# Optimization experiments

Hardware: AMD Instinct MI355X
Metric: run time of the kernel (lower is better)

## Reference

```python
import jax, jax.numpy as jnp
import numpy as np

N = 40000          # nodes
E = 640000         # edges
D_IN, D_HID, D_EMB, D_OUT = 128, 128, 64, 2


def glorot(key, shape):
    lim = np.sqrt(6.0 / (shape[0] + shape[1]))
    return jax.random.uniform(key, shape, jnp.float32, -lim, lim)


def setup_inputs() -> dict:
    key = jax.random.key(0)
    ks = jax.random.split(key, 8)
    x = jax.random.normal(ks[0], (N, D_IN), jnp.float32)
    edge_index = jax.random.randint(ks[1], (2, E), 0, N, dtype=jnp.int64)
    # GCNConv weights stored as [in, out]; biases zero-init per PyG default
    W1 = glorot(ks[2], (D_IN, D_HID));  b1 = jnp.zeros((D_HID,), jnp.float32)
    W2 = glorot(ks[3], (D_HID, D_HID)); b2 = jnp.zeros((D_HID,), jnp.float32)
    W3 = glorot(ks[4], (D_HID, D_EMB)); b3 = jnp.zeros((D_EMB,), jnp.float32)
    Wout = glorot(ks[5], (D_EMB, D_OUT)); bout = jnp.zeros((D_OUT,), jnp.float32)
    return {"x": x, "edge_index": edge_index,
            "W1": W1, "b1": b1, "W2": W2, "b2": b2,
            "W3": W3, "b3": b3, "Wout": Wout, "bout": bout}


def _gcn_norm(edge_index, n):
    # add self loops, compute symmetric normalization d^-1/2[src] * d^-1/2[dst]
    loop = jnp.arange(n, dtype=edge_index.dtype)
    src = jnp.concatenate([edge_index[0], loop])
    dst = jnp.concatenate([edge_index[1], loop])
    deg = jax.ops.segment_sum(jnp.ones_like(dst, dtype=jnp.float32), dst,
                              num_segments=n)
    dinv = jax.lax.rsqrt(deg)                      # deg >= 1 due to self-loops
    dinv = jnp.where(jnp.isinf(dinv), 0.0, dinv)
    return src, dst, dinv[src] * dinv[dst]


def gcn_conv(x, src, dst, norm, W, b):
    h = x @ W                                      # [N, out]
    msg = h[src] * norm[:, None]                   # gather + scale  [E+N, out]
    return jax.ops.segment_sum(msg, dst, num_segments=x.shape[0]) + b


def reference(x, edge_index, W1, b1, W2, b2, W3, b3, Wout, bout):
    n = x.shape[0]
    src, dst, norm = _gcn_norm(edge_index, n)      # cached=True: computed once
    h = jax.nn.relu(gcn_conv(x, src, dst, norm, W1, b1))   # dropout is identity in eval
    h = jax.nn.relu(gcn_conv(h, src, dst, norm, W2, b2))
    h = gcn_conv(h, src, dst, norm, W3, b3)
    out = h @ Wout + bout
    return (out, h)
```

## Files before the change

kernel.cpp:

```cpp
#include <hip/hip_runtime.h>
#include <hip/hip_bf16.h>

#define NN 40000
#define NE 640000

typedef unsigned int u32;
typedef unsigned short u16;
typedef __attribute__((ext_vector_type(8))) short bf16x8;
typedef __attribute__((ext_vector_type(4))) float f32x4;

__device__ float g_wf[512];
__device__ u16   g_wp[40960];
__device__ int   g_cnt[NN];
__device__ int   g_cur[NN];
__device__ int   g_rowptr[NN + 1];
__device__ float g_dinv[NN];
__device__ int   g_csrc[NE];
__device__ int   g_bsum[64];
__device__ u16   g_ha[(size_t)NN * 128];
__device__ u16   g_hb[(size_t)NN * 128];
__device__ u16   g_hb2[(size_t)NN * 128];

#define OFF_B1 0
#define OFF_B2 128
#define OFF_B3 256
#define OFF_WO 320
#define OFF_BO 448
#define WP_W1 0
#define WP_W2 16384
#define WP_W3 32768

__device__ __forceinline__ float b2f(u16 v){ return __uint_as_float(((u32)v) << 16); }
__device__ __forceinline__ float blo(u32 u){ return __uint_as_float(u << 16); }
__device__ __forceinline__ float bhi(u32 u){ return __uint_as_float(u & 0xffff0000u); }
__device__ __forceinline__ u32 f2bf(float f){
  u32 u = __float_as_uint(f);
  return (u + 0x7fffu + ((u >> 16) & 1u)) >> 16;
}
__device__ __forceinline__ int clampi(int v, int lo, int hi){ return v < lo ? lo : (v > hi ? hi : v); }
__device__ __forceinline__ u16 ldbf(const void* p, int idx, int f32){
  return f32 ? (u16)f2bf(((const float*)p)[idx]) : ((const u16*)p)[idx];
}
__device__ __forceinline__ float ldf(const void* p, int idx, int f32){
  return f32 ? ((const float*)p)[idx] : b2f(((const u16*)p)[idx]);
}

__device__ __forceinline__ int detect_xf32(const u16* __restrict__ xf){
  int i = ((int)threadIdx.x & 63) * 64;
  u16 v = xf[2 * i];
  int e = (v >> 7) & 0xff;
  int pass = (v == 0 || (e >= 100 && e <= 140)) ? 1 : 0;
  return (__popcll(__ballot(pass)) < 32) ? 1 : 0;
}
__device__ __forceinline__ int detect_estride(const int* __restrict__ ei){
  int i = ((int)threadIdx.x & 63) * 64;
  int pass = (ei[2 * i + 1] == 0) ? 1 : 0;
  return (__popcll(__ballot(pass)) >= 32) ? 2 : 1;
}

__global__ __launch_bounds__(256) void k_prep(const void* xin, const int* __restrict__ ei,
                                              const void* w1, const void* b1,
                                              const void* w2, const void* b2, const void* w3,
                                              const void* b3, const void* wo, const void* bo){
  int xf32 = detect_xf32((const u16*)xin);
  int strd = detect_estride(ei);
  int T = (int)blockIdx.x * 256 + (int)threadIdx.x;
  if (T < 640000){
    if (xf32){
      const float4* p = (const float4*)xin + (size_t)T * 2;
      float4 a = p[0], b = p[1];
      uint4 o;
      o.x = f2bf(a.x) | (f2bf(a.y) << 16);
      o.y = f2bf(a.z) | (f2bf(a.w) << 16);
      o.z = f2bf(b.x) | (f2bf(b.y) << 16);
      o.w = f2bf(b.z) | (f2bf(b.w) << 16);
      ((uint4*)g_ha)[T] = o;
    } else {
      ((uint4*)g_ha)[T] = ((const uint4*)xin)[T];
    }
    int d = clampi(ei[(size_t)(NE + T) * strd], 0, NN - 1);
    atomicAdd(&g_cnt[d], 1);
  } else if (T < 680960){
    int local = T - 640000;
    int J, dstbase, l; const void* src;
    if (local < 16384){ J = 128; src = w1; dstbase = WP_W1; l = local; }
    else if (local < 32768){ J = 128; src = w2; dstbase = WP_W2; l = local - 16384; }
    else { J = 64; src = w3; dstbase = WP_W3; l = local - 32768; }
    int chunk = l >> 9, within = l & 511;
    int nbw = J / 16;
    int kb = chunk / nbw, nb = chunk % nbw;
    int lane = within >> 3, j = within & 7;
    int q = lane >> 4, n = lane & 15;
    int k = kb * 32 + q * 8 + j;
    int col = nb * 16 + n;
    g_wp[dstbase + l] = ldbf(src, k * J + col, xf32);
  } else if (T < 681410){
    int l = T - 680960;
    if (l < 128)      g_wf[OFF_B1 + l] = ldf(b1, l, xf32);
    else if (l < 256) g_wf[OFF_B2 + l - 128] = ldf(b2, l - 128, xf32);
    else if (l < 320) g_wf[OFF_B3 + l - 256] = ldf(b3, l - 256, xf32);
    else if (l < 448) g_wf[OFF_WO + l - 320] = ldf(wo, l - 320, xf32);
    else              g_wf[OFF_BO + l - 448] = ldf(bo, l - 448, xf32);
  }
}

__global__ __launch_bounds__(1024) void k_scan1(){
  int t = (int)threadIdx.x;
  int b = (int)blockIdx.x;
  int i = b * 1024 + t;
  int v = (i < NN) ? g_cnt[i] : 0;
  int lane = t & 63, wv = t >> 6;
  int x = v;
#pragma unroll
  for (int ofs = 1; ofs < 64; ofs <<= 1){
    int y = __shfl_up(x, ofs, 64);
    if (lane >= ofs) x += y;
  }
  __shared__ int wsum[16];
  if (lane == 63) wsum[wv] = x;
  __syncthreads();
  if (t < 16){
    int s = wsum[t];
#pragma unroll
    for (int ofs = 1; ofs < 16; ofs <<= 1){
      int y = __shfl_up(s, ofs, 64);
      if (t >= ofs) s += y;
    }
    wsum[t] = s;
  }
  __syncthreads();
  int pre = (wv == 0) ? 0 : wsum[wv - 1];
  int incl = x + pre;
  if (i < NN){
    g_rowptr[i] = incl - v;
    g_dinv[i] = rsqrtf((float)(v + 1));
  }
  if (t == 1023) g_bsum[b] = incl;
}

__global__ __launch_bounds__(1024) void k_scan3(){
  __shared__ int pre;
  int t = (int)threadIdx.x;
  if (t < 64){
    int v = (t < 40) ? g_bsum[t] : 0;
    int s = v;
#pragma unroll
    for (int ofs = 1; ofs < 64; ofs <<= 1){
      int y = __shfl_up(s, ofs, 64);
      if (t >= ofs) s += y;
    }
    if (t == (int)blockIdx.x) pre = s - v;
    if (blockIdx.x == 0 && t == 39) g_rowptr[NN] = s;
  }
  __syncthreads();
  int i = (int)blockIdx.x * 1024 + t;
  if (i < NN) g_rowptr[i] += pre;
}

__global__ __launch_bounds__(256) void k_fillgemm(const int* __restrict__ ei){
  int bid = (int)blockIdx.x;
  if (bid < 2500){
    int strd = detect_estride(ei);
    int e = bid * 256 + (int)threadIdx.x;
    if (e < NE){
      int d = clampi(ei[(size_t)(NE + e) * strd], 0, NN - 1);
      int s = clampi(ei[(size_t)e * strd], 0, NN - 1);
      int pos = clampi(g_rowptr[d] + atomicAdd(&g_cur[d], 1), 0, NE - 1);
      g_csrc[pos] = s;
    }
  } else {
    constexpr int J = 128;
    constexpr int NB = J / 16;
    int tid = (int)threadIdx.x;
    int wave = tid >> 6, lane = tid & 63;
    int q = lane >> 4, n = lane & 15;
    int m0 = (bid - 2500) * 64 + wave * 16;
    f32x4 acc[NB];
#pragma unroll
    for (int nb = 0; nb < NB; ++nb) acc[nb] = (f32x4){0.f, 0.f, 0.f, 0.f};
    const u16* arow = g_ha + (size_t)(m0 + n) * 128 + q * 8;
#pragma unroll
    for (int kb = 0; kb < 4; ++kb){
      bf16x8 a = *(const bf16x8*)(arow + kb * 32);
      const u16* wbase = g_wp + WP_W1 + (kb * NB) * 512 + lane * 8;
#pragma unroll
      for (int nb = 0; nb < NB; ++nb){
        bf16x8 w = *(const bf16x8*)(wbase + nb * 512);
        acc[nb] = __builtin_amdgcn_mfma_f32_16x16x32_bf16(a, w, acc[nb], 0, 0, 0);
      }
    }
    u16* crow = g_hb + (size_t)(m0 + q * 4) * J + n;
#pragma unroll
    for (int r = 0; r < 4; ++r){
      float di = g_dinv[m0 + q * 4 + r];
#pragma unroll
      for (int nb = 0; nb < NB; ++nb)
        crow[(size_t)r * J + nb * 16] = (u16)f2bf(acc[nb][r] * di);
    }
  }
}

#define ACC8(P) do { \
    a0 += blo((P).x); a1 += bhi((P).x); \
    a2 += blo((P).y); a3 += bhi((P).y); \
    a4 += blo((P).z); a5 += bhi((P).z); \
    a6 += blo((P).w); a7 += bhi((P).w); } while (0)

template<int JOUT, bool SWAP, bool ZCLR>
__global__ __launch_bounds__(256, 4) void k_agggemm(int boff, int wpoff){
  constexpr int LSTRIDE = 136;
  __shared__ u16 tile[16 * LSTRIDE];
  const u16* __restrict__ src = SWAP ? g_hb2 : g_hb;
  u16* __restrict__ dst = SWAP ? g_hb : g_hb2;
  int tid = (int)threadIdx.x;
  int gt = (int)blockIdx.x * 256 + tid;
  if (ZCLR){ if (gt < NN){ g_cnt[gt] = 0; g_cur[gt] = 0; } }
  int wid = gt >> 4;
  int rt = tid >> 4;
  int lane = tid & 15;
  int cc = lane * 8;
  float di = g_dinv[wid];
  int beg = g_rowptr[wid], end = g_rowptr[wid + 1];
  uint4 ps = *(const uint4*)(src + (size_t)wid * 128 + cc);
  float a0 = 0.f, a1 = 0.f, a2 = 0.f, a3 = 0.f, a4 = 0.f, a5 = 0.f, a6 = 0.f, a7 = 0.f;
  for (int e = beg; e < end; e += 8){
    int s0, s1, s2, s3, s4, s5, s6, s7;
    {
      int last = end - 1;
#define LDS_IDX(T) clampi(g_csrc[(e + T < last) ? (e + T) : last], 0, NN - 1)
      s0 = LDS_IDX(0); s1 = LDS_IDX(1); s2 = LDS_IDX(2); s3 = LDS_IDX(3);
      s4 = LDS_IDX(4); s5 = LDS_IDX(5); s6 = LDS_IDX(6); s7 = LDS_IDX(7);
#undef LDS_IDX
    }
    uint4 p0 = *(const uint4*)(src + (size_t)s0 * 128 + cc);
    uint4 p1 = *(const uint4*)(src + (size_t)s1 * 128 + cc);
    uint4 p2 = *(const uint4*)(src + (size_t)s2 * 128 + cc);
    uint4 p3 = *(const uint4*)(src + (size_t)s3 * 128 + cc);
    uint4 p4 = *(const uint4*)(src + (size_t)s4 * 128 + cc);
    uint4 p5 = *(const uint4*)(src + (size_t)s5 * 128 + cc);
    uint4 p6 = *(const uint4*)(src + (size_t)s6 * 128 + cc);
    uint4 p7 = *(const uint4*)(src + (size_t)s7 * 128 + cc);
    int nv = end - e;
    ACC8(p0);
    if (nv > 1) ACC8(p1);
    if (nv > 2) ACC8(p2);
    if (nv > 3) ACC8(p3);
    if (nv > 4) ACC8(p4);
    if (nv > 5) ACC8(p5);
    if (nv > 6) ACC8(p6);
    if (nv > 7) ACC8(p7);
  }
  ACC8(ps);
  a0 = a0 * di + g_wf[boff + cc];
  a1 = a1 * di + g_wf[boff + cc + 1];
  a2 = a2 * di + g_wf[boff + cc + 2];
  a3 = a3 * di + g_wf[boff + cc + 3];
  a4 = a4 * di + g_wf[boff + cc + 4];
  a5 = a5 * di + g_wf[boff + cc + 5];
  a6 = a6 * di + g_wf[boff + cc + 6];
  a7 = a7 * di + g_wf[boff + cc + 7];
  a0 = fmaxf(a0, 0.f); a1 = fmaxf(a1, 0.f); a2 = fmaxf(a2, 0.f); a3 = fmaxf(a3, 0.f);
  a4 = fmaxf(a4, 0.f); a5 = fmaxf(a5, 0.f); a6 = fmaxf(a6, 0.f); a7 = fmaxf(a7, 0.f);
  {
    uint4 o;
    o.x = f2bf(a0) | (f2bf(a1) << 16);
    o.y = f2bf(a2) | (f2bf(a3) << 16);
    o.z = f2bf(a4) | (f2bf(a5) << 16);
    o.w = f2bf(a6) | (f2bf(a7) << 16);
    *(uint4*)&tile[rt * LSTRIDE + cc] = o;
  }
  __syncthreads();
  constexpr int NBF = JOUT / 16;
  constexpr int NBW = NBF / 4;
  int wave = tid >> 6, l64 = tid & 63;
  int q = l64 >> 4, n = l64 & 15;
  f32x4 acc[NBW];
#pragma unroll
  for (int j = 0; j < NBW; ++j) acc[j] = (f32x4){0.f, 0.f, 0.f, 0.f};
#pragma unroll
  for (int kb = 0; kb < 4; ++kb){
    bf16x8 a = *(const bf16x8*)&tile[n * LSTRIDE + q * 8 + kb * 32];
#pragma unroll
    for (int j = 0; j < NBW; ++j){
      int nb = wave * NBW + j;
      bf16x8 w = *(const bf16x8*)(g_wp + wpoff + (kb * NBF + nb) * 512 + l64 * 8);
      acc[j] = __builtin_amdgcn_mfma_f32_16x16x32_bf16(a, w, acc[j], 0, 0, 0);
    }
  }
  int m0 = (int)blockIdx.x * 16;
#pragma unroll
  for (int r = 0; r < 4; ++r){
    float dr = g_dinv[m0 + q * 4 + r];
#pragma unroll
    for (int j = 0; j < NBW; ++j){
      int nb = wave * NBW + j;
      dst[(size_t)(m0 + q * 4 + r) * JOUT + nb * 16 + n] = (u16)f2bf(acc[j][r] * dr);
    }
  }
}

template<int J, bool RELU>
__global__ __launch_bounds__(256, 4) void k_agg(int boff, float* __restrict__ h3, float* __restrict__ outp){
  constexpr int LPR = J / 8;
  int gt = (int)blockIdx.x * 256 + (int)threadIdx.x;
  int wid = gt / LPR;
  int lane = (int)threadIdx.x & (LPR - 1);
  if (wid >= NN) return;
  int cc = lane * 8;
  const u16* __restrict__ hb = g_hb;
  float di = g_dinv[wid];
  int beg = g_rowptr[wid], end = g_rowptr[wid + 1];
  uint4 ps = *(const uint4*)(hb + (size_t)wid * J + cc);
  float a0 = 0.f, a1 = 0.f, a2 = 0.f, a3 = 0.f, a4 = 0.f, a5 = 0.f, a6 = 0.f, a7 = 0.f;
  for (int e = beg; e < end; e += 8){
    int s0, s1, s2, s3, s4, s5, s6, s7;
    {
      int last = end - 1;
#define LDS_IDX(T) clampi(g_csrc[(e + T < last) ? (e + T) : last], 0, NN - 1)
      s0 = LDS_IDX(0); s1 = LDS_IDX(1); s2 = LDS_IDX(2); s3 = LDS_IDX(3);
      s4 = LDS_IDX(4); s5 = LDS_IDX(5); s6 = LDS_IDX(6); s7 = LDS_IDX(7);
#undef LDS_IDX
    }
    uint4 p0 = *(const uint4*)(hb + (size_t)s0 * J + cc);
    uint4 p1 = *(const uint4*)(hb + (size_t)s1 * J + cc);
    uint4 p2 = *(const uint4*)(hb + (size_t)s2 * J + cc);
    uint4 p3 = *(const uint4*)(hb + (size_t)s3 * J + cc);
    uint4 p4 = *(const uint4*)(hb + (size_t)s4 * J + cc);
    uint4 p5 = *(const uint4*)(hb + (size_t)s5 * J + cc);
    uint4 p6 = *(const uint4*)(hb + (size_t)s6 * J + cc);
    uint4 p7 = *(const uint4*)(hb + (size_t)s7 * J + cc);
    int nv = end - e;
    ACC8(p0);
    if (nv > 1) ACC8(p1);
    if (nv > 2) ACC8(p2);
    if (nv > 3) ACC8(p3);
    if (nv > 4) ACC8(p4);
    if (nv > 5) ACC8(p5);
    if (nv > 6) ACC8(p6);
    if (nv > 7) ACC8(p7);
  }
  ACC8(ps);
  a0 = a0 * di + g_wf[boff + cc];
  a1 = a1 * di + g_wf[boff + cc + 1];
  a2 = a2 * di + g_wf[boff + cc + 2];
  a3 = a3 * di + g_wf[boff + cc + 3];
  a4 = a4 * di + g_wf[boff + cc + 4];
  a5 = a5 * di + g_wf[boff + cc + 5];
  a6 = a6 * di + g_wf[boff + cc + 6];
  a7 = a7 * di + g_wf[boff + cc + 7];
  if (RELU){
    a0 = fmaxf(a0, 0.f); a1 = fmaxf(a1, 0.f); a2 = fmaxf(a2, 0.f); a3 = fmaxf(a3, 0.f);
    a4 = fmaxf(a4, 0.f); a5 = fmaxf(a5, 0.f); a6 = fmaxf(a6, 0.f); a7 = fmaxf(a7, 0.f);
  }
  *(float4*)(h3 + (size_t)wid * 64 + cc)     = make_float4(a0, a1, a2, a3);
  *(float4*)(h3 + (size_t)wid * 64 + cc + 4) = make_float4(a4, a5, a6, a7);
  float o0 = a0 * g_wf[OFF_WO + (cc + 0) * 2] + a1 * g_wf[OFF_WO + (cc + 1) * 2]
           + a2 * g_wf[OFF_WO + (cc + 2) * 2] + a3 * g_wf[OFF_WO + (cc + 3) * 2]
           + a4 * g_wf[OFF_WO + (cc + 4) * 2] + a5 * g_wf[OFF_WO + (cc + 5) * 2]
           + a6 * g_wf[OFF_WO + (cc + 6) * 2] + a7 * g_wf[OFF_WO + (cc + 7) * 2];
  float o1 = a0 * g_wf[OFF_WO + (cc + 0) * 2 + 1] + a1 * g_wf[OFF_WO + (cc + 1) * 2 + 1]
           + a2 * g_wf[OFF_WO + (cc + 2) * 2 + 1] + a3 * g_wf[OFF_WO + (cc + 3) * 2 + 1]
           + a4 * g_wf[OFF_WO + (cc + 4) * 2 + 1] + a5 * g_wf[OFF_WO + (cc + 5) * 2 + 1]
           + a6 * g_wf[OFF_WO + (cc + 6) * 2 + 1] + a7 * g_wf[OFF_WO + (cc + 7) * 2 + 1];
#pragma unroll
  for (int m = 1; m < 8; m <<= 1){
    o0 += __shfl_xor(o0, m, 64);
    o1 += __shfl_xor(o1, m, 64);
  }
  if (lane == 0){
    *(float2*)(outp + (size_t)wid * 2) =
      make_float2(o0 + g_wf[OFF_BO], o1 + g_wf[OFF_BO + 1]);
  }
}

extern "C" void kernel_launch(void* const* d_in, const int* in_sizes, int n_in,
                              void* d_out, int out_size, void* d_ws, size_t ws_size,
                              hipStream_t stream){
  const int* ei = (const int*)d_in[1];
  float* out = (float*)d_out;
  float* h3  = out + (size_t)NN * 2;

  k_prep<<<2662, 256, 0, stream>>>(d_in[0], ei, d_in[2], d_in[3], d_in[4], d_in[5],
                                   d_in[6], d_in[7], d_in[8], d_in[9]);
  k_scan1<<<40, 1024, 0, stream>>>();
  k_scan3<<<40, 1024, 0, stream>>>();
  k_fillgemm<<<3125, 256, 0, stream>>>(ei);

  k_agggemm<128, false, true><<<2500, 256, 0, stream>>>(OFF_B1, WP_W2);
  k_agggemm<64, true, false><<<2500, 256, 0, stream>>>(OFF_B2, WP_W3);
  k_agg<64, false><<<1250, 256, 0, stream>>>(OFF_B3, h3, out);
}
```

Measured before the change: 229.5 us.

## Bucket CSR edges by source-node range to improve gather cache locality

Edges are now counted and placed into a CSR keyed by (source bucket, destination), with four buckets of 10000 source nodes each. The aggregation kernels walk the four buckets in turn, so waves running at the same time tend to gather from the same quarter of the feature table, which should raise L2 hit rates on the random row gathers. The cost is a prefix scan four times larger, a serial per-block prefix over block sums, four row-pointer lookups per node, and shorter per-bucket edge runs that waste more of the 8-wide unrolled gather slots.

After: 235.4 us. +2.6%, slower.

```diff
diff --git a/kernel.cpp b/kernel.cpp
--- a/kernel.cpp
+++ b/kernel.cpp
@@ -3,6 +3,9 @@
 
 #define NN 40000
 #define NE 640000
+#define NB4 4
+#define BDIV 10000
+#define NN4 (NN * NB4)
 
 typedef unsigned int u32;
 typedef unsigned short u16;
@@ -11,12 +14,12 @@
 
 __device__ float g_wf[512];
 __device__ u16   g_wp[40960];
-__device__ int   g_cnt[NN];
-__device__ int   g_cur[NN];
-__device__ int   g_rowptr[NN + 1];
+__device__ int   g_cnt[NN4];
+__device__ int   g_cur[NN4];
+__device__ int   g_rowptr[NN4 + 1];
 __device__ float g_dinv[NN];
 __device__ int   g_csrc[NE];
-__device__ int   g_bsum[64];
+__device__ int   g_bsum[160];
 __device__ u16   g_ha[(size_t)NN * 128];
 __device__ u16   g_hb[(size_t)NN * 128];
 __device__ u16   g_hb2[(size_t)NN * 128];
@@ -79,7 +82,8 @@
       ((uint4*)g_ha)[T] = ((const uint4*)xin)[T];
     }
     int d = clampi(ei[(size_t)(NE + T) * strd], 0, NN - 1);
-    atomicAdd(&g_cnt[d], 1);
+    int s = clampi(ei[(size_t)T * strd], 0, NN - 1);
+    atomicAdd(&g_cnt[(s / BDIV) * NN + d], 1);
   } else if (T < 680960){
     int local = T - 640000;
     int J, dstbase, l; const void* src;
@@ -108,7 +112,7 @@
   int t = (int)threadIdx.x;
   int b = (int)blockIdx.x;
   int i = b * 1024 + t;
-  int v = (i < NN) ? g_cnt[i] : 0;
+  int v = (i < NN4) ? g_cnt[i] : 0;
   int lane = t & 63, wv = t >> 6;
   int x = v;
 #pragma unroll
@@ -131,30 +135,31 @@
   __syncthreads();
   int pre = (wv == 0) ? 0 : wsum[wv - 1];
   int incl = x + pre;
-  if (i < NN){
-    g_rowptr[i] = incl - v;
-    g_dinv[i] = rsqrtf((float)(v + 1));
-  }
+  if (i < NN4) g_rowptr[i] = incl - v;
   if (t == 1023) g_bsum[b] = incl;
 }
 
 __global__ __launch_bounds__(1024) void k_scan3(){
   __shared__ int pre;
   int t = (int)threadIdx.x;
-  if (t < 64){
-    int v = (t < 40) ? g_bsum[t] : 0;
-    int s = v;
-#pragma unroll
-    for (int ofs = 1; ofs < 64; ofs <<= 1){
-      int y = __shfl_up(s, ofs, 64);
-      if (t >= ofs) s += y;
-    }
-    if (t == (int)blockIdx.x) pre = s - v;
-    if (blockIdx.x == 0 && t == 39) g_rowptr[NN] = s;
+  int b = (int)blockIdx.x;
+  if (t == 0){
+    int s = 0;
+    for (int j = 0; j < b; ++j) s += g_bsum[j];
+    pre = s;
+    if (b == 156){
+      int tot = s;
+      for (int j = b; j < 157; ++j) tot += g_bsum[j];
+      g_rowptr[NN4] = tot;
+    }
   }
   __syncthreads();
-  int i = (int)blockIdx.x * 1024 + t;
-  if (i < NN) g_rowptr[i] += pre;
+  int i = b * 1024 + t;
+  if (i < NN4) g_rowptr[i] += pre;
+  if (i < NN){
+    int deg = g_cnt[i] + g_cnt[NN + i] + g_cnt[2 * NN + i] + g_cnt[3 * NN + i];
+    g_dinv[i] = rsqrtf((float)(deg + 1));
+  }
 }
 
 __global__ __launch_bounds__(256) void k_fillgemm(const int* __restrict__ ei){
@@ -165,7 +170,8 @@
     if (e < NE){
       int d = clampi(ei[(size_t)(NE + e) * strd], 0, NN - 1);
       int s = clampi(ei[(size_t)e * strd], 0, NN - 1);
-      int pos = clampi(g_rowptr[d] + atomicAdd(&g_cur[d], 1), 0, NE - 1);
+      int v = (s / BDIV) * NN + d;
+      int pos = clampi(g_rowptr[v] + atomicAdd(&g_cur[v], 1), 0, NE - 1);
       g_csrc[pos] = s;
     }
   } else {
@@ -214,41 +220,44 @@
   u16* __restrict__ dst = SWAP ? g_hb : g_hb2;
   int tid = (int)threadIdx.x;
   int gt = (int)blockIdx.x * 256 + tid;
-  if (ZCLR){ if (gt < NN){ g_cnt[gt] = 0; g_cur[gt] = 0; } }
+  if (ZCLR){ if (gt < NN4){ g_cnt[gt] = 0; g_cur[gt] = 0; } }
   int wid = gt >> 4;
   int rt = tid >> 4;
   int lane = tid & 15;
   int cc = lane * 8;
   float di = g_dinv[wid];
-  int beg = g_rowptr[wid], end = g_rowptr[wid + 1];
   uint4 ps = *(const uint4*)(src + (size_t)wid * 128 + cc);
   float a0 = 0.f, a1 = 0.f, a2 = 0.f, a3 = 0.f, a4 = 0.f, a5 = 0.f, a6 = 0.f, a7 = 0.f;
-  for (int e = beg; e < end; e += 8){
-    int s0, s1, s2, s3, s4, s5, s6, s7;
-    {
-      int last = end - 1;
+#pragma unroll
+  for (int bk = 0; bk < NB4; ++bk){
+    int beg = g_rowptr[bk * NN + wid], end = g_rowptr[bk * NN + wid + 1];
+    for (int e = beg; e < end; e += 8){
+      int s0, s1, s2, s3, s4, s5, s6, s7;
+      {
+        int last = end - 1;
 #define LDS_IDX(T) clampi(g_csrc[(e + T < last) ? (e + T) : last], 0, NN - 1)
-      s0 = LDS_IDX(0); s1 = LDS_IDX(1); s2 = LDS_IDX(2); s3 = LDS_IDX(3);
-      s4 = LDS_IDX(4); s5 = LDS_IDX(5); s6 = LDS_IDX(6); s7 = LDS_IDX(7);
+        s0 = LDS_IDX(0); s1 = LDS_IDX(1); s2 = LDS_IDX(2); s3 = LDS_IDX(3);
+        s4 = LDS_IDX(4); s5 = LDS_IDX(5); s6 = LDS_IDX(6); s7 = LDS_IDX(7);
 #undef LDS_IDX
-    }
-    uint4 p0 = *(const uint4*)(src + (size_t)s0 * 128 + cc);
-    uint4 p1 = *(const uint4*)(src + (size_t)s1 * 128 + cc);
-    uint4 p2 = *(const uint4*)(src + (size_t)s2 * 128 + cc);
-    uint4 p3 = *(const uint4*)(src + (size_t)s3 * 128 + cc);
-    uint4 p4 = *(const uint4*)(src + (size_t)s4 * 128 + cc);
-    uint4 p5 = *(const uint4*)(src + (size_t)s5 * 128 + cc);
-    uint4 p6 = *(const uint4*)(src + (size_t)s6 * 128 + cc);
-    uint4 p7 = *(const uint4*)(src + (size_t)s7 * 128 + cc);
-    int nv = end - e;
-    ACC8(p0);
-    if (nv > 1) ACC8(p1);
-    if (nv > 2) ACC8(p2);
-    if (nv > 3) ACC8(p3);
-    if (nv > 4) ACC8(p4);
-    if (nv > 5) ACC8(p5);
-    if (nv > 6) ACC8(p6);
-    if (nv > 7) ACC8(p7);
+      }
+      uint4 p0 = *(const uint4*)(src + (size_t)s0 * 128 + cc);
+      uint4 p1 = *(const uint4*)(src + (size_t)s1 * 128 + cc);
+      uint4 p2 = *(const uint4*)(src + (size_t)s2 * 128 + cc);
+      uint4 p3 = *(const uint4*)(src + (size_t)s3 * 128 + cc);
+      uint4 p4 = *(const uint4*)(src + (size_t)s4 * 128 + cc);
+      uint4 p5 = *(const uint4*)(src + (size_t)s5 * 128 + cc);
+      uint4 p6 = *(const uint4*)(src + (size_t)s6 * 128 + cc);
+      uint4 p7 = *(const uint4*)(src + (size_t)s7 * 128 + cc);
+      int nv = end - e;
+      ACC8(p0);
+      if (nv > 1) ACC8(p1);
+      if (nv > 2) ACC8(p2);
+      if (nv > 3) ACC8(p3);
+      if (nv > 4) ACC8(p4);
+      if (nv > 5) ACC8(p5);
+      if (nv > 6) ACC8(p6);
+      if (nv > 7) ACC8(p7);
+    }
   }
   ACC8(ps);
   a0 = a0 * di + g_wf[boff + cc];
@@ -299,45 +308,48 @@
   }
 }
 
-template<int J, bool RELU>
+template<bool RELU>
 __global__ __launch_bounds__(256, 4) void k_agg(int boff, float* __restrict__ h3, float* __restrict__ outp){
-  constexpr int LPR = J / 8;
-  int gt = (int)blockIdx.x * 256 + (int)threadIdx.x;
-  int wid = gt / LPR;
-  int lane = (int)threadIdx.x & (LPR - 1);
+  int tid = (int)threadIdx.x;
+  int gt = (int)blockIdx.x * 256 + tid;
+  int wid = gt >> 3;
+  int lane = tid & 7;
   if (wid >= NN) return;
   int cc = lane * 8;
   const u16* __restrict__ hb = g_hb;
   float di = g_dinv[wid];
-  int beg = g_rowptr[wid], end = g_rowptr[wid + 1];
-  uint4 ps = *(const uint4*)(hb + (size_t)wid * J + cc);
+  uint4 ps = *(const uint4*)(hb + (size_t)wid * 64 + cc);
   float a0 = 0.f, a1 = 0.f, a2 = 0.f, a3 = 0.f, a4 = 0.f, a5 = 0.f, a6 = 0.f, a7 = 0.f;
-  for (int e = beg; e < end; e += 8){
-    int s0, s1, s2, s3, s4, s5, s6, s7;
-    {
-      int last = end - 1;
+#pragma unroll
+  for (int bk = 0; bk < NB4; ++bk){
+    int beg = g_rowptr[bk * NN + wid], end = g_rowptr[bk * NN + wid + 1];
+    for (int e = beg; e < end; e += 8){
+      int s0, s1, s2, s3, s4, s5, s6, s7;
+      {
+        int last = end - 1;
 #define LDS_IDX(T) clampi(g_csrc[(e + T < last) ? (e + T) : last], 0, NN - 1)
-      s0 = LDS_IDX(0); s1 = LDS_IDX(1); s2 = LDS_IDX(2); s3 = LDS_IDX(3);
-      s4 = LDS_IDX(4); s5 = LDS_IDX(5); s6 = LDS_IDX(6); s7 = LDS_IDX(7);
+        s0 = LDS_IDX(0); s1 = LDS_IDX(1); s2 = LDS_IDX(2); s3 = LDS_IDX(3);
+        s4 = LDS_IDX(4); s5 = LDS_IDX(5); s6 = LDS_IDX(6); s7 = LDS_IDX(7);
 #undef LDS_IDX
-    }
-    uint4 p0 = *(const uint4*)(hb + (size_t)s0 * J + cc);
-    uint4 p1 = *(const uint4*)(hb + (size_t)s1 * J + cc);
-    uint4 p2 = *(const uint4*)(hb + (size_t)s2 * J + cc);
-    uint4 p3 = *(const uint4*)(hb + (size_t)s3 * J + cc);
-    uint4 p4 = *(const uint4*)(hb + (size_t)s4 * J + cc);
-    uint4 p5 = *(const uint4*)(hb + (size_t)s5 * J + cc);
-    uint4 p6 = *(const uint4*)(hb + (size_t)s6 * J + cc);
-    uint4 p7 = *(const uint4*)(hb + (size_t)s7 * J + cc);
-    int nv = end - e;
-    ACC8(p0);
-    if (nv > 1) ACC8(p1);
-    if (nv > 2) ACC8(p2);
-    if (nv > 3) ACC8(p3);
-    if (nv > 4) ACC8(p4);
-    if (nv > 5) ACC8(p5);
-    if (nv > 6) ACC8(p6);
-    if (nv > 7) ACC8(p7);
+      }
+      uint4 p0 = *(const uint4*)(hb + (size_t)s0 * 64 + cc);
+      uint4 p1 = *(const uint4*)(hb + (size_t)s1 * 64 + cc);
+      uint4 p2 = *(const uint4*)(hb + (size_t)s2 * 64 + cc);
+      uint4 p3 = *(const uint4*)(hb + (size_t)s3 * 64 + cc);
+      uint4 p4 = *(const uint4*)(hb + (size_t)s4 * 64 + cc);
+      uint4 p5 = *(const uint4*)(hb + (size_t)s5 * 64 + cc);
+      uint4 p6 = *(const uint4*)(hb + (size_t)s6 * 64 + cc);
+      uint4 p7 = *(const uint4*)(hb + (size_t)s7 * 64 + cc);
+      int nv = end - e;
+      ACC8(p0);
+      if (nv > 1) ACC8(p1);
+      if (nv > 2) ACC8(p2);
+      if (nv > 3) ACC8(p3);
+      if (nv > 4) ACC8(p4);
+      if (nv > 5) ACC8(p5);
+      if (nv > 6) ACC8(p6);
+      if (nv > 7) ACC8(p7);
+    }
   }
   ACC8(ps);
   a0 = a0 * di + g_wf[boff + cc];
@@ -382,11 +394,11 @@
 
   k_prep<<<2662, 256, 0, stream>>>(d_in[0], ei, d_in[2], d_in[3], d_in[4], d_in[5],
                                    d_in[6], d_in[7], d_in[8], d_in[9]);
-  k_scan1<<<40, 1024, 0, stream>>>();
-  k_scan3<<<40, 1024, 0, stream>>>();
+  k_scan1<<<157, 1024, 0, stream>>>();
+  k_scan3<<<157, 1024, 0, stream>>>();
   k_fillgemm<<<3125, 256, 0, stream>>>(ei);
 
   k_agggemm<128, false, true><<<2500, 256, 0, stream>>>(OFF_B1, WP_W2);
   k_agggemm<64, true, false><<<2500, 256, 0, stream>>>(OFF_B2, WP_W3);
-  k_agg<64, false><<<1250, 256, 0, stream>>>(OFF_B3, h3, out);
-}
+  k_agg<false><<<1250, 256, 0, stream>>>(OFF_B3, h3, out);
+}
```
